# Kernel tuning notes

Hardware: AMD Instinct MI355X
Metric: run time of the kernel (lower is better)

The kernel has to match this reference:

```python
import jax, jax.numpy as jnp
import numpy as np

TAU_RA = 30.0
K3 = 2.0
DT = 0.1


def setup_inputs() -> dict:
    key = jax.random.key(0)
    I_in = jax.random.normal(key, (8, 4096, 2048), dtype=jnp.float32)
    return {"I_in": I_in}


def reference(I_in):
    # I_in: (batch, time, neurons)
    # finite-difference derivative; first step uses I_in[:,0]/dt
    dI = jnp.concatenate(
        [I_in[:, :1, :], I_in[:, 1:, :] - I_in[:, :-1, :]], axis=1
    ) / DT
    # drive term: k3*|dI|*dt/tau, decay a = 1 - dt/tau
    a = 1.0 - DT / TAU_RA
    drive = (K3 * DT / TAU_RA) * jnp.abs(dI)  # (B, T, N)
    # linear recurrence I_RA[t] = a * I_RA[t-1] + drive[t], I_RA[-1] = 0
    drive_t = jnp.swapaxes(drive, 0, 1)  # (T, B, N) for scan over time

    def step(state, u):
        new = a * state + u
        return new, new

    init = jnp.zeros(drive_t.shape[1:], dtype=I_in.dtype)
    _, outs = jax.lax.scan(step, init, drive_t)
    return jnp.swapaxes(outs, 0, 1)  # (B, T, N)
```

## Files before the change

kernel.cpp:

```cpp
#include <hip/hip_runtime.h>


constexpr int Bb = 8;
constexpr int Tn = 4096;
constexpr int Nn = 2048;
constexpr int UNROLL = 32;

__global__ __launch_bounds__(64) void ra_filter_kernel(
    const float* __restrict__ in, float* __restrict__ out) {
    const int gid = blockIdx.x * 64 + threadIdx.x;
    const int b = gid >> 11;
    const int n = gid & (Nn - 1);

    const size_t base = (size_t)b * Tn * Nn + n;
    const float* p = in + base;
    float* q = out + base;

    const float a = (float)(1.0 - 0.1 / 30.0);
    const float c = (float)(2.0 / 30.0);

    float xa[UNROLL], xb[UNROLL];
    float prev = 0.0f, state = 0.0f;

#pragma unroll
    for (int u = 0; u < UNROLL; ++u)
        xa[u] = __builtin_nontemporal_load(p + (size_t)u * Nn);

    for (int t0 = 0; t0 < Tn; t0 += 2 * UNROLL) {
#pragma unroll
        for (int u = 0; u < UNROLL; ++u)
            xb[u] = __builtin_nontemporal_load(p + (size_t)(t0 + UNROLL + u) * Nn);

#pragma unroll
        for (int u = 0; u < UNROLL; ++u) {
            float x = xa[u];
            float d = x - prev;
            prev = x;
            state = fmaf(a, state, c * fabsf(d));
            xa[u] = state;
        }
#pragma unroll
        for (int u = 0; u < UNROLL; ++u)
            __builtin_nontemporal_store(xa[u], q + (size_t)(t0 + u) * Nn);

        if (t0 + 2 * UNROLL < Tn) {
#pragma unroll
            for (int u = 0; u < UNROLL; ++u)
                xa[u] = __builtin_nontemporal_load(p + (size_t)(t0 + 2 * UNROLL + u) * Nn);
        }

#pragma unroll
        for (int u = 0; u < UNROLL; ++u) {
            float x = xb[u];
            float d = x - prev;
            prev = x;
            state = fmaf(a, state, c * fabsf(d));
            xb[u] = state;
        }
#pragma unroll
        for (int u = 0; u < UNROLL; ++u)
            __builtin_nontemporal_store(xb[u], q + (size_t)(t0 + UNROLL + u) * Nn);
    }
}

extern "C" void kernel_launch(void* const* d_in, const int* in_sizes, int n_in,
                              void* d_out, int out_size, void* d_ws, size_t ws_size,
                              hipStream_t stream) {
    const float* in = (const float*)d_in[0];
    float* out = (float*)d_out;

    const int chains = Bb * Nn;
    dim3 grid(chains / 64), block(64);
    hipLaunchKernelGGL(ra_filter_kernel, grid, block, 0, stream, in, out);
}
```

Before: 464.9 us.

## Split time into segments with two-pass carry propagation for more parallelism

Each chain's time axis is split into 16 segments handled by separate wavefronts in one block. A first pass computes each segment's end state from zero initial state. Carries are combined through shared memory using the segment decay factor a^256, and a second pass recomputes the segment with the correct carry and writes output. This raises wave-level parallelism far beyond one wave per CU, at the cost of reading the input twice and a block barrier.

```diff
diff --git a/kernel.cpp b/kernel.cpp
--- a/kernel.cpp
+++ b/kernel.cpp
@@ -1,65 +1,103 @@
 #include <hip/hip_runtime.h>
 
 
-constexpr int Bb = 8;
-constexpr int Tn = 4096;
-constexpr int Nn = 2048;
-constexpr int UNROLL = 32;
+constexpr int Bb  = 8;
+constexpr int Tn  = 4096;
+constexpr int Nn  = 2048;
+constexpr int SEG = 16;
+constexpr int L   = Tn / SEG;
+constexpr int U   = 16;
 
-__global__ __launch_bounds__(64) void ra_filter_kernel(
+__global__ __launch_bounds__(64 * SEG) void ra_filter2_kernel(
     const float* __restrict__ in, float* __restrict__ out) {
-    const int gid = blockIdx.x * 64 + threadIdx.x;
-    const int b = gid >> 11;
-    const int n = gid & (Nn - 1);
+    const int lane = threadIdx.x & 63;
+    const int s    = threadIdx.x >> 6;
+    const int nb   = blockIdx.x & (Nn / 64 - 1);
+    const int b    = blockIdx.x >> 5;
+    const int n    = nb * 64 + lane;
+
+    const float a = 0.99666666666666667f;
+    const float c = 0.06666666666666667f;
+    float A = a;
+#pragma unroll
+    for (int i = 0; i < 8; ++i) A = A * A;
 
     const size_t base = (size_t)b * Tn * Nn + n;
-    const float* p = in + base;
-    float* q = out + base;
+    const int t0 = s * L;
+    const float* p = in  + base + (size_t)t0 * Nn;
+    float*       q = out + base + (size_t)t0 * Nn;
 
-    const float a = (float)(1.0 - 0.1 / 30.0);
-    const float c = (float)(2.0 / 30.0);
+    float E = 0.0f;
+    if (s < SEG - 1) {
+        float prev = (t0 == 0) ? 0.0f : p[-(ptrdiff_t)Nn];
+        float st = 0.0f;
+        float xa[U], xb[U];
+#pragma unroll
+        for (int u = 0; u < U; ++u) xa[u] = p[(size_t)u * Nn];
+        for (int tt = 0; tt < L; tt += 2 * U) {
+#pragma unroll
+            for (int u = 0; u < U; ++u) xb[u] = p[(size_t)(tt + U + u) * Nn];
+#pragma unroll
+            for (int u = 0; u < U; ++u) {
+                float x = xa[u];
+                st = fmaf(a, st, c * fabsf(x - prev));
+                prev = x;
+            }
+            if (tt + 2 * U < L) {
+#pragma unroll
+                for (int u = 0; u < U; ++u) xa[u] = p[(size_t)(tt + 2 * U + u) * Nn];
+            }
+#pragma unroll
+            for (int u = 0; u < U; ++u) {
+                float x = xb[u];
+                st = fmaf(a, st, c * fabsf(x - prev));
+                prev = x;
+            }
+        }
+        E = st;
+    }
 
-    float xa[UNROLL], xb[UNROLL];
-    float prev = 0.0f, state = 0.0f;
+    __shared__ float lds_E[SEG][64];
+    lds_E[s][lane] = E;
+    __syncthreads();
 
+    float carry = 0.0f;
+    for (int j = 0; j < s; ++j) carry = fmaf(A, carry, lds_E[j][lane]);
+
+    {
+        float prev = (t0 == 0) ? 0.0f : p[-(ptrdiff_t)Nn];
+        float st = carry;
+        float xa[U], xb[U];
 #pragma unroll
-    for (int u = 0; u < UNROLL; ++u)
-        xa[u] = __builtin_nontemporal_load(p + (size_t)u * Nn);
-
-    for (int t0 = 0; t0 < Tn; t0 += 2 * UNROLL) {
+        for (int u = 0; u < U; ++u) xa[u] = p[(size_t)u * Nn];
+        for (int tt = 0; tt < L; tt += 2 * U) {
 #pragma unroll
-        for (int u = 0; u < UNROLL; ++u)
-            xb[u] = __builtin_nontemporal_load(p + (size_t)(t0 + UNROLL + u) * Nn);
-
+            for (int u = 0; u < U; ++u) xb[u] = p[(size_t)(tt + U + u) * Nn];
 #pragma unroll
-        for (int u = 0; u < UNROLL; ++u) {
-            float x = xa[u];
-            float d = x - prev;
-            prev = x;
-            state = fmaf(a, state, c * fabsf(d));
-            xa[u] = state;
+            for (int u = 0; u < U; ++u) {
+                float x = xa[u];
+                st = fmaf(a, st, c * fabsf(x - prev));
+                prev = x;
+                xa[u] = st;
+            }
+#pragma unroll
+            for (int u = 0; u < U; ++u)
+                __builtin_nontemporal_store(xa[u], q + (size_t)(tt + u) * Nn);
+            if (tt + 2 * U < L) {
+#pragma unroll
+                for (int u = 0; u < U; ++u) xa[u] = p[(size_t)(tt + 2 * U + u) * Nn];
+            }
+#pragma unroll
+            for (int u = 0; u < U; ++u) {
+                float x = xb[u];
+                st = fmaf(a, st, c * fabsf(x - prev));
+                prev = x;
+                xb[u] = st;
+            }
+#pragma unroll
+            for (int u = 0; u < U; ++u)
+                __builtin_nontemporal_store(xb[u], q + (size_t)(tt + U + u) * Nn);
         }
-#pragma unroll
-        for (int u = 0; u < UNROLL; ++u)
-            __builtin_nontemporal_store(xa[u], q + (size_t)(t0 + u) * Nn);
-
-        if (t0 + 2 * UNROLL < Tn) {
-#pragma unroll
-            for (int u = 0; u < UNROLL; ++u)
-                xa[u] = __builtin_nontemporal_load(p + (size_t)(t0 + 2 * UNROLL + u) * Nn);
-        }
-
-#pragma unroll
-        for (int u = 0; u < UNROLL; ++u) {
-            float x = xb[u];
-            float d = x - prev;
-            prev = x;
-            state = fmaf(a, state, c * fabsf(d));
-            xb[u] = state;
-        }
-#pragma unroll
-        for (int u = 0; u < UNROLL; ++u)
-            __builtin_nontemporal_store(xb[u], q + (size_t)(t0 + UNROLL + u) * Nn);
     }
 }
 
@@ -69,7 +107,6 @@
     const float* in = (const float*)d_in[0];
     float* out = (float*)d_out;
 
-    const int chains = Bb * Nn;
-    dim3 grid(chains / 64), block(64);
-    hipLaunchKernelGGL(ra_filter_kernel, grid, block, 0, stream, in, out);
+    dim3 grid(Bb * (Nn / 64)), block(64 * SEG);
+    hipLaunchKernelGGL(ra_filter2_kernel, grid, block, 0, stream, in, out);
 }
```

New measurement: 465.3 us. About the same (+0.1%).
